# Kernel tuning notes

Hardware: AMD Instinct MI355X
Metric: run time of the kernel (lower is better)

Reference implementation:

```python
import jax, jax.numpy as jnp
import numpy as np
from jax import lax

B, T, H, NC, SKEL, GEN = 512, 256, 512, 512, 256, 16


def setup_inputs() -> dict:
    key = jax.random.key(0)
    ks = jax.random.split(key, 16)
    s = 0.05
    return {
        "inputs": jax.random.randint(ks[0], (B, T), 0, NC),  # teacher-forcing ids (unused, training=False)
        "note_encoded": jax.random.normal(ks[1], (B, SKEL), jnp.float32),
        "genre_cond": jax.random.normal(ks[2], (B, GEN), jnp.float32),
        # hidden_fc
        "W_hid": jax.random.normal(ks[3], (H, SKEL + GEN), jnp.float32) * s,
        "b_hid": jnp.zeros((H,), jnp.float32),
        # embedding table
        "emb": jax.random.normal(ks[4], (NC, H), jnp.float32) * s,
        # gru1 (torch GRUCell layout: gates [r, z, n] stacked along dim 0)
        "W_ih1": jax.random.normal(ks[5], (3 * H, H), jnp.float32) * s,
        "W_hh1": jax.random.normal(ks[6], (3 * H, H), jnp.float32) * s,
        "b_ih1": jnp.zeros((3 * H,), jnp.float32),
        "b_hh1": jnp.zeros((3 * H,), jnp.float32),
        # gru2
        "W_ih2": jax.random.normal(ks[7], (3 * H, H), jnp.float32) * s,
        "W_hh2": jax.random.normal(ks[8], (3 * H, H), jnp.float32) * s,
        "b_ih2": jnp.zeros((3 * H,), jnp.float32),
        "b_hh2": jnp.zeros((3 * H,), jnp.float32),
        # out_fc Linear
        "W_out": jax.random.normal(ks[9], (NC, H), jnp.float32) * s,
        "b_out": jnp.zeros((NC,), jnp.float32),
    }


def gru_cell(x, h, W_ih, W_hh, b_ih, b_hh):
    # torch.nn.GRUCell math
    gi = x @ W_ih.T + b_ih          # [B, 3H]
    gh = h @ W_hh.T + b_hh          # [B, 3H]
    i_r, i_z, i_n = jnp.split(gi, 3, axis=-1)
    h_r, h_z, h_n = jnp.split(gh, 3, axis=-1)
    r = jax.nn.sigmoid(i_r + h_r)
    z = jax.nn.sigmoid(i_z + h_z)
    n = jnp.tanh(i_n + r * h_n)
    return (1.0 - z) * n + z * h


def reference(inputs, note_encoded, genre_cond, W_hid, b_hid, emb,
              W_ih1, W_hh1, b_ih1, b_hh1, W_ih2, W_hh2, b_ih2, b_hh2,
              W_out, b_out):
    batch = note_encoded.shape[0]
    hidden = jnp.concatenate([note_encoded, genre_cond], axis=-1)  # use_genre_cond=True
    h1_init = hidden @ W_hid.T + b_hid                              # [B, H]
    h2_init = jnp.zeros_like(h1_init)  # overwritten at step 0 (hx[1] = hx[0])
    tok0 = jnp.zeros((batch,), jnp.int32)
    sample_keys = jax.random.split(jax.random.key(42), T)

    def step(carry, xs):
        h1, h2, tok = carry
        i, k = xs
        x = emb[tok]                                    # embedding lookup [B, H]
        h1 = gru_cell(x, h1, W_ih1, W_hh1, b_ih1, b_hh1)
        h2_prev = jnp.where(i == 0, h1, h2)             # hx[1] = hx[0] at i==0
        h2 = gru_cell(h1, h2_prev, W_ih2, W_hh2, b_ih2, b_hh2)
        logits = h2 @ W_out.T + b_out                   # [B, NC]
        # Categorical(softmax(logits)/temp) renormalizes => temp is a no-op.
        tok = jax.random.categorical(k, jax.nn.log_softmax(logits, axis=-1)).astype(jnp.int32)
        return (h1, h2, tok), (logits, tok)

    _, (logits_seq, tok_seq) = lax.scan(step, (h1_init, h2_init, tok0),
                                        (jnp.arange(T), sample_keys))
    code_outs = jnp.swapaxes(logits_seq, 0, 1)  # [B, T, NC]
    pred_outs = jnp.swapaxes(tok_seq, 0, 1)     # [B, T]
    return code_outs, pred_outs
```

## Files before the change

kernel.cpp:

```cpp
#include <hip/hip_runtime.h>
#include <stdint.h>

#define BB 512
#define TT 256
#define HH 512
#define NCC 512
#define KIN 272

typedef float v2f __attribute__((ext_vector_type(2)));

__device__ __forceinline__ void tf_round(uint32_t &x0, uint32_t &x1, int r) {
  x0 += x1;
  x1 = (x1 << r) | (x1 >> (32 - r));
  x1 ^= x0;
}

__device__ __forceinline__ void threefry2x32(uint32_t k0, uint32_t k1,
                                             uint32_t c0, uint32_t c1,
                                             uint32_t &o0, uint32_t &o1) {
  uint32_t ks2 = k0 ^ k1 ^ 0x1BD11BDAu;
  uint32_t x0 = c0 + k0, x1 = c1 + k1;
  tf_round(x0, x1, 13); tf_round(x0, x1, 15); tf_round(x0, x1, 26); tf_round(x0, x1, 6);
  x0 += k1;  x1 += ks2 + 1u;
  tf_round(x0, x1, 17); tf_round(x0, x1, 29); tf_round(x0, x1, 16); tf_round(x0, x1, 24);
  x0 += ks2; x1 += k0 + 2u;
  tf_round(x0, x1, 13); tf_round(x0, x1, 15); tf_round(x0, x1, 26); tf_round(x0, x1, 6);
  x0 += k0;  x1 += k1 + 3u;
  tf_round(x0, x1, 17); tf_round(x0, x1, 29); tf_round(x0, x1, 16); tf_round(x0, x1, 24);
  x0 += k1;  x1 += ks2 + 4u;
  tf_round(x0, x1, 13); tf_round(x0, x1, 15); tf_round(x0, x1, 26); tf_round(x0, x1, 6);
  x0 += ks2; x1 += k0 + 5u;
  o0 = x0; o1 = x1;
}

__global__ void __launch_bounds__(256) init_kernel(
    const float* __restrict__ note, const float* __restrict__ genre,
    const float* __restrict__ Whid, const float* __restrict__ bhid,
    const float* __restrict__ emb,
    float* __restrict__ h1T, float* __restrict__ xT, int* __restrict__ tok) {
  int b = blockIdx.x;
  int tid = threadIdx.x;
  __shared__ double u[KIN];
  if (tid < 256) u[tid] = (double)note[b * 256 + tid];
  if (tid < 16)  u[256 + tid] = (double)genre[b * 16 + tid];
  if (tid == 0)  tok[b] = 0;
  __syncthreads();
  for (int j = tid; j < HH; j += 256) {
    double acc = 0.0;
    const float* w = Whid + (size_t)j * KIN;
    #pragma unroll 4
    for (int k = 0; k < KIN; ++k) acc = fma(u[k], (double)w[k], acc);
    h1T[(size_t)j * BB + b] = (float)(acc + (double)bhid[j]);
    xT[(size_t)j * BB + b]  = emb[j];
  }
}

#define CT 8
#define BT 64
#define KT 32
__global__ void __launch_bounds__(256) gru_kernel(
    const float* __restrict__ Wih, const float* __restrict__ Whh,
    const float* __restrict__ bih, const float* __restrict__ bhh,
    const float* __restrict__ hprevT, float* __restrict__ houtT,
    const float* __restrict__ xT) {
  __shared__ float xs[KT][BT];
  __shared__ float hs[KT][BT];
  __shared__ float ws[6][4][KT][2];

  int tid  = threadIdx.x;
  int lane = tid & 63;
  int wv   = tid >> 6;
  int j0   = blockIdx.x * CT;
  int b0   = blockIdx.y * BT;

  int krow = tid >> 3;
  int bq   = (tid & 7) * 8;
  const float* xsrc = xT     + (size_t)krow * BB + b0 + bq;
  const float* hsrc = hprevT + (size_t)krow * BB + b0 + bq;

  auto wsrcf = [&](int f) -> const float* {
    int kq = f & 7, row = f >> 3;
    int cc = row & 1, pr = (row >> 1) & 3, g = row >> 3;
    const float* base = (g < 3) ? Wih : Whh;
    int gg = (g < 3) ? g : g - 3;
    return base + ((size_t)gg * HH + j0 + pr * 2 + cc) * HH + kq * 4;
  };
  auto wdstf = [&](int f) -> float* {
    int kq = f & 7, row = f >> 3;
    int cc = row & 1, pr = (row >> 1) & 3, g = row >> 3;
    return &ws[g][pr][kq * 4][cc];
  };
  bool has2 = (tid < 128);
  const float* wsrc1 = wsrcf(tid);
  const float* wsrc2 = has2 ? wsrcf(tid + 256) : wsrc1;
  float* wdst1 = wdstf(tid);
  float* wdst2 = has2 ? wdstf(tid + 256) : wdst1;

  v2f acc[6];
  #pragma unroll
  for (int g = 0; g < 6; ++g) { acc[g][0] = 0.0f; acc[g][1] = 0.0f; }

  float4 px0 = *(const float4*)(xsrc);
  float4 px1 = *(const float4*)(xsrc + 4);
  float4 ph0 = *(const float4*)(hsrc);
  float4 ph1 = *(const float4*)(hsrc + 4);
  float4 pw1 = *(const float4*)(wsrc1);
  float4 pw2 = *(const float4*)(wsrc2);

  for (int k0 = 0; k0 < HH; k0 += KT) {
    __syncthreads();
    *(float4*)&xs[krow][bq]     = px0;
    *(float4*)&xs[krow][bq + 4] = px1;
    *(float4*)&hs[krow][bq]     = ph0;
    *(float4*)&hs[krow][bq + 4] = ph1;
    wdst1[0] = pw1.x; wdst1[2] = pw1.y; wdst1[4] = pw1.z; wdst1[6] = pw1.w;
    if (has2) { wdst2[0] = pw2.x; wdst2[2] = pw2.y; wdst2[4] = pw2.z; wdst2[6] = pw2.w; }
    __syncthreads();

    if (k0 + KT < HH) {
      xsrc += (size_t)KT * BB; hsrc += (size_t)KT * BB;
      wsrc1 += KT; wsrc2 += KT;
      px0 = *(const float4*)(xsrc);
      px1 = *(const float4*)(xsrc + 4);
      ph0 = *(const float4*)(hsrc);
      ph1 = *(const float4*)(hsrc + 4);
      pw1 = *(const float4*)(wsrc1);
      pw2 = *(const float4*)(wsrc2);
    }

    #pragma unroll 8
    for (int kk = 0; kk < KT; kk += 2) {
      float xa = xs[kk][lane],     ha = hs[kk][lane];
      float xb = xs[kk + 1][lane], hb = hs[kk + 1][lane];
      v2f xa2 = {xa, xa}, xb2 = {xb, xb};
      v2f ha2 = {ha, ha}, hb2 = {hb, hb};
      #pragma unroll
      for (int g = 0; g < 3; ++g) {
        float4 wq = *(const float4*)&ws[g][wv][kk][0];
        v2f lo = {wq.x, wq.y}, hi = {wq.z, wq.w};
        acc[g] = __builtin_elementwise_fma(xa2, lo, acc[g]);
        acc[g] = __builtin_elementwise_fma(xb2, hi, acc[g]);
      }
      #pragma unroll
      for (int g = 3; g < 6; ++g) {
        float4 wq = *(const float4*)&ws[g][wv][kk][0];
        v2f lo = {wq.x, wq.y}, hi = {wq.z, wq.w};
        acc[g] = __builtin_elementwise_fma(ha2, lo, acc[g]);
        acc[g] = __builtin_elementwise_fma(hb2, hi, acc[g]);
      }
    }
  }

  int b = b0 + lane;
  #pragma unroll
  for (int ci = 0; ci < 2; ++ci) {
    int j = j0 + wv * 2 + ci;
    double ir  = (double)acc[0][ci] + (double)bih[j];
    double iz  = (double)acc[1][ci] + (double)bih[HH + j];
    double inn = (double)acc[2][ci] + (double)bih[2 * HH + j];
    double hr  = (double)acc[3][ci] + (double)bhh[j];
    double hz  = (double)acc[4][ci] + (double)bhh[HH + j];
    double hn  = (double)acc[5][ci] + (double)bhh[2 * HH + j];
    double r = 1.0 / (1.0 + exp(-(ir + hr)));
    double z = 1.0 / (1.0 + exp(-(iz + hz)));
    double n = tanh(inn + r * hn);
    double hp = (double)hprevT[(size_t)j * BB + b];
    houtT[(size_t)j * BB + b] = (float)((1.0 - z) * n + z * hp);
  }
}

__global__ void __launch_bounds__(256) sample_kernel(
    const float* __restrict__ Wout, const float* __restrict__ bout,
    const float* __restrict__ h2T, float* __restrict__ out0,
    float* __restrict__ out1, int* __restrict__ tok, int t,
    const float* __restrict__ emb, float* __restrict__ xT) {
  __shared__ double hsh[2][HH];
  __shared__ double rs[2][256];
  __shared__ int    ri[2][256];
  int tid = threadIdx.x;
  int b0 = blockIdx.x * 2;

  for (int i = tid; i < 2 * HH; i += 256)
    hsh[i >> 9][i & 511] = (double)h2T[(size_t)(i & 511) * BB + b0 + (i >> 9)];
  __syncthreads();

  uint32_t k1t, k2t;
  threefry2x32(0u, 42u, 0u, (uint32_t)t, k1t, k2t);

  double sbest[2]; int ibest[2];
  #pragma unroll
  for (int half = 0; half < 2; ++half) {
    int cc = tid + half * 256;
    double acc[2] = {0, 0};
    const float* w = Wout + (size_t)cc * HH;
    for (int k = 0; k < HH; k += 4) {
      float4 wv = *(const float4*)(w + k);
      #pragma unroll
      for (int i = 0; i < 2; ++i) {
        acc[i] = fma(hsh[i][k + 0], (double)wv.x, acc[i]);
        acc[i] = fma(hsh[i][k + 1], (double)wv.y, acc[i]);
        acc[i] = fma(hsh[i][k + 2], (double)wv.z, acc[i]);
        acc[i] = fma(hsh[i][k + 3], (double)wv.w, acc[i]);
      }
    }
    double bo = (double)bout[cc];
    #pragma unroll
    for (int i = 0; i < 2; ++i) {
      int b = b0 + i;
      double lg = acc[i] + bo;
      out0[((size_t)b * TT + t) * NCC + cc] = (float)lg;
      uint32_t o0, o1;
      threefry2x32(k1t, k2t, 0u, (uint32_t)(b * NCC + cc), o0, o1);
      uint32_t bits = o0 ^ o1;
      uint32_t ub = bits >> 9;
      float uf;
      if (ub == 0u) uf = 1.17549435e-38f;
      else          uf = __uint_as_float(0x3f800000u | ub) - 1.0f;
      double g = -log(-log((double)uf));
      double s = lg + g;
      if (half == 0) { sbest[i] = s; ibest[i] = cc; }
      else if (s > sbest[i]) { sbest[i] = s; ibest[i] = cc; }
    }
  }
  #pragma unroll
  for (int i = 0; i < 2; ++i) { rs[i][tid] = sbest[i]; ri[i][tid] = ibest[i]; }
  __syncthreads();
  for (int stride = 128; stride > 0; stride >>= 1) {
    if (tid < stride) {
      #pragma unroll
      for (int i = 0; i < 2; ++i) {
        double so = rs[i][tid + stride]; int io = ri[i][tid + stride];
        double sm = rs[i][tid];          int im = ri[i][tid];
        if (so > sm || (so == sm && io < im)) { rs[i][tid] = so; ri[i][tid] = io; }
      }
    }
    __syncthreads();
  }
  if (tid < 2) {
    int b = b0 + tid;
    int idx = ri[tid][0];
    tok[b] = idx;
    out1[(size_t)b * TT + t] = (float)idx;
  }
  #pragma unroll
  for (int i = 0; i < 2; ++i) {
    int row = ri[i][0];
    int b = b0 + i;
    for (int k = tid; k < HH; k += 256)
      xT[(size_t)k * BB + b] = emb[(size_t)row * HH + k];
  }
}

extern "C" void kernel_launch(void* const* d_in, const int* in_sizes, int n_in,
                              void* d_out, int out_size, void* d_ws, size_t ws_size,
                              hipStream_t stream) {
  const float* note  = (const float*)d_in[1];
  const float* genre = (const float*)d_in[2];
  const float* Whid  = (const float*)d_in[3];
  const float* bhid  = (const float*)d_in[4];
  const float* emb   = (const float*)d_in[5];
  const float* Wih1  = (const float*)d_in[6];
  const float* Whh1  = (const float*)d_in[7];
  const float* bih1  = (const float*)d_in[8];
  const float* bhh1  = (const float*)d_in[9];
  const float* Wih2  = (const float*)d_in[10];
  const float* Whh2  = (const float*)d_in[11];
  const float* bih2  = (const float*)d_in[12];
  const float* bhh2  = (const float*)d_in[13];
  const float* Wout  = (const float*)d_in[14];
  const float* bout  = (const float*)d_in[15];

  float* out0 = (float*)d_out;
  float* out1 = out0 + (size_t)BB * TT * NCC;

  char* wsp = (char*)d_ws;
  float* h1a = (float*)wsp; wsp += (size_t)BB * HH * sizeof(float);
  float* h1b = (float*)wsp; wsp += (size_t)BB * HH * sizeof(float);
  float* h2a = (float*)wsp; wsp += (size_t)BB * HH * sizeof(float);
  float* h2b = (float*)wsp; wsp += (size_t)BB * HH * sizeof(float);
  float* xT  = (float*)wsp; wsp += (size_t)HH * BB * sizeof(float);
  int* tok = (int*)wsp;

  init_kernel<<<BB, 256, 0, stream>>>(note, genre, Whid, bhid, emb, h1a, xT, tok);

  float* c1 = h1a;
  float* c2 = h2a;
  dim3 ggrid(HH / CT, BB / BT);
  for (int t = 0; t < TT; ++t) {
    float* n1 = (c1 == h1a) ? h1b : h1a;
    float* n2 = (c2 == h2a) ? h2b : h2a;
    gru_kernel<<<ggrid, 256, 0, stream>>>(Wih1, Whh1, bih1, bhh1, c1, n1, xT);
    const float* hsrc2 = (t == 0) ? (const float*)n1 : (const float*)c2;
    gru_kernel<<<ggrid, 256, 0, stream>>>(Wih2, Whh2, bih2, bhh2, hsrc2, n2, n1);
    sample_kernel<<<BB / 2, 256, 0, stream>>>(Wout, bout, n2, out0, out1, tok, t,
                                              emb, xT);
    c1 = n1;
    c2 = n2;
  }
}
```

Baseline: 34.59 ms.

## Repack GRU weights per column pair and read them directly from global memory

Adds a repack kernel that lays out the six GRU gate weight matrices as interleaved column pairs, contiguous along k, once per layer at the start of each call. The GRU kernel drops its shared-memory weight staging and reads packed weights straight from global memory with wave-uniform addresses, which should turn into scalar or broadcast loads. This removes the LDS weight stores and their bank traffic. In exchange, weight loads now depend on cache latency inside the inner loop, and two repack launches plus extra workspace are added to every forward call.

```diff
diff --git a/kernel.cpp b/kernel.cpp
--- a/kernel.cpp
+++ b/kernel.cpp
@@ -31,6 +31,20 @@
   tf_round(x0, x1, 13); tf_round(x0, x1, 15); tf_round(x0, x1, 26); tf_round(x0, x1, 6);
   x0 += ks2; x1 += k0 + 5u;
   o0 = x0; o1 = x1;
+}
+
+__global__ void __launch_bounds__(256) repack_kernel(
+    const float* __restrict__ Wih, const float* __restrict__ Whh,
+    float* __restrict__ wpack) {
+  int idx = blockIdx.x * 256 + threadIdx.x;
+  int c   = idx & 1;
+  int k   = (idx >> 1) & 511;
+  int gcp = idx >> 10;
+  int g   = gcp % 6;
+  int cp  = gcp / 6;
+  const float* W = (g < 3) ? Wih : Whh;
+  int gg = (g < 3) ? g : g - 3;
+  wpack[idx] = W[((size_t)(gg * HH + cp * 2 + c)) * HH + k];
 }
 
 __global__ void __launch_bounds__(256) init_kernel(
@@ -55,46 +69,29 @@
   }
 }
 
-#define CT 8
-#define BT 64
-#define KT 32
+#define GBT 64
+#define GKT 32
 __global__ void __launch_bounds__(256) gru_kernel(
-    const float* __restrict__ Wih, const float* __restrict__ Whh,
+    const float* __restrict__ wpack,
     const float* __restrict__ bih, const float* __restrict__ bhh,
     const float* __restrict__ hprevT, float* __restrict__ houtT,
     const float* __restrict__ xT) {
-  __shared__ float xs[KT][BT];
-  __shared__ float hs[KT][BT];
-  __shared__ float ws[6][4][KT][2];
+  __shared__ float xs[GKT][GBT];
+  __shared__ float hs[GKT][GBT];
 
   int tid  = threadIdx.x;
   int lane = tid & 63;
-  int wv   = tid >> 6;
-  int j0   = blockIdx.x * CT;
-  int b0   = blockIdx.y * BT;
-
-  int krow = tid >> 3;
-  int bq   = (tid & 7) * 8;
-  const float* xsrc = xT     + (size_t)krow * BB + b0 + bq;
-  const float* hsrc = hprevT + (size_t)krow * BB + b0 + bq;
-
-  auto wsrcf = [&](int f) -> const float* {
-    int kq = f & 7, row = f >> 3;
-    int cc = row & 1, pr = (row >> 1) & 3, g = row >> 3;
-    const float* base = (g < 3) ? Wih : Whh;
-    int gg = (g < 3) ? g : g - 3;
-    return base + ((size_t)gg * HH + j0 + pr * 2 + cc) * HH + kq * 4;
-  };
-  auto wdstf = [&](int f) -> float* {
-    int kq = f & 7, row = f >> 3;
-    int cc = row & 1, pr = (row >> 1) & 3, g = row >> 3;
-    return &ws[g][pr][kq * 4][cc];
-  };
-  bool has2 = (tid < 128);
-  const float* wsrc1 = wsrcf(tid);
-  const float* wsrc2 = has2 ? wsrcf(tid + 256) : wsrc1;
-  float* wdst1 = wdstf(tid);
-  float* wdst2 = has2 ? wdstf(tid + 256) : wdst1;
+  int wv   = __builtin_amdgcn_readfirstlane(tid >> 6);
+  int j0   = blockIdx.x * 8;
+  int b0   = blockIdx.y * GBT;
+  int cp   = blockIdx.x * 4 + wv;
+
+  const float* wbase = wpack + (size_t)cp * (6 * 512 * 2);
+
+  int kr = tid >> 3;
+  int bq = (tid & 7) * 8;
+  const float* xsrc = xT     + (size_t)kr * BB + b0 + bq;
+  const float* hsrc = hprevT + (size_t)kr * BB + b0 + bq;
 
   v2f acc[6];
   #pragma unroll
@@ -104,46 +101,42 @@
   float4 px1 = *(const float4*)(xsrc + 4);
   float4 ph0 = *(const float4*)(hsrc);
   float4 ph1 = *(const float4*)(hsrc + 4);
-  float4 pw1 = *(const float4*)(wsrc1);
-  float4 pw2 = *(const float4*)(wsrc2);
-
-  for (int k0 = 0; k0 < HH; k0 += KT) {
+
+  for (int k0 = 0; k0 < HH; k0 += GKT) {
     __syncthreads();
-    *(float4*)&xs[krow][bq]     = px0;
-    *(float4*)&xs[krow][bq + 4] = px1;
-    *(float4*)&hs[krow][bq]     = ph0;
-    *(float4*)&hs[krow][bq + 4] = ph1;
-    wdst1[0] = pw1.x; wdst1[2] = pw1.y; wdst1[4] = pw1.z; wdst1[6] = pw1.w;
-    if (has2) { wdst2[0] = pw2.x; wdst2[2] = pw2.y; wdst2[4] = pw2.z; wdst2[6] = pw2.w; }
+    *(float4*)&xs[kr][bq]     = px0;
+    *(float4*)&xs[kr][bq + 4] = px1;
+    *(float4*)&hs[kr][bq]     = ph0;
+    *(float4*)&hs[kr][bq + 4] = ph1;
     __syncthreads();
 
-    if (k0 + KT < HH) {
-      xsrc += (size_t)KT * BB; hsrc += (size_t)KT * BB;
-      wsrc1 += KT; wsrc2 += KT;
+    if (k0 + GKT < HH) {
+      xsrc += (size_t)GKT * BB;
+      hsrc += (size_t)GKT * BB;
       px0 = *(const float4*)(xsrc);
       px1 = *(const float4*)(xsrc + 4);
       ph0 = *(const float4*)(hsrc);
       ph1 = *(const float4*)(hsrc + 4);
-      pw1 = *(const float4*)(wsrc1);
-      pw2 = *(const float4*)(wsrc2);
-    }
-
-    #pragma unroll 8
-    for (int kk = 0; kk < KT; kk += 2) {
+    }
+
+    const float* wk0 = wbase + (size_t)k0 * 2;
+    #pragma unroll
+    for (int kk = 0; kk < GKT; kk += 2) {
       float xa = xs[kk][lane],     ha = hs[kk][lane];
       float xb = xs[kk + 1][lane], hb = hs[kk + 1][lane];
       v2f xa2 = {xa, xa}, xb2 = {xb, xb};
       v2f ha2 = {ha, ha}, hb2 = {hb, hb};
+      const float* wk = wk0 + kk * 2;
       #pragma unroll
       for (int g = 0; g < 3; ++g) {
-        float4 wq = *(const float4*)&ws[g][wv][kk][0];
+        float4 wq = *(const float4*)(wk + g * 1024);
         v2f lo = {wq.x, wq.y}, hi = {wq.z, wq.w};
         acc[g] = __builtin_elementwise_fma(xa2, lo, acc[g]);
         acc[g] = __builtin_elementwise_fma(xb2, hi, acc[g]);
       }
       #pragma unroll
       for (int g = 3; g < 6; ++g) {
-        float4 wq = *(const float4*)&ws[g][wv][kk][0];
+        float4 wq = *(const float4*)(wk + g * 1024);
         v2f lo = {wq.x, wq.y}, hi = {wq.z, wq.w};
         acc[g] = __builtin_elementwise_fma(ha2, lo, acc[g]);
         acc[g] = __builtin_elementwise_fma(hb2, hi, acc[g]);
@@ -279,19 +272,23 @@
   float* h2a = (float*)wsp; wsp += (size_t)BB * HH * sizeof(float);
   float* h2b = (float*)wsp; wsp += (size_t)BB * HH * sizeof(float);
   float* xT  = (float*)wsp; wsp += (size_t)HH * BB * sizeof(float);
+  float* wp1 = (float*)wsp; wsp += (size_t)256 * 6 * 512 * 2 * sizeof(float);
+  float* wp2 = (float*)wsp; wsp += (size_t)256 * 6 * 512 * 2 * sizeof(float);
   int* tok = (int*)wsp;
 
+  repack_kernel<<<12288, 256, 0, stream>>>(Wih1, Whh1, wp1);
+  repack_kernel<<<12288, 256, 0, stream>>>(Wih2, Whh2, wp2);
   init_kernel<<<BB, 256, 0, stream>>>(note, genre, Whid, bhid, emb, h1a, xT, tok);
 
   float* c1 = h1a;
   float* c2 = h2a;
-  dim3 ggrid(HH / CT, BB / BT);
+  dim3 ggrid(HH / 8, BB / GBT);
   for (int t = 0; t < TT; ++t) {
     float* n1 = (c1 == h1a) ? h1b : h1a;
     float* n2 = (c2 == h2a) ? h2b : h2a;
-    gru_kernel<<<ggrid, 256, 0, stream>>>(Wih1, Whh1, bih1, bhh1, c1, n1, xT);
+    gru_kernel<<<ggrid, 256, 0, stream>>>(wp1, bih1, bhh1, c1, n1, xT);
     const float* hsrc2 = (t == 0) ? (const float*)n1 : (const float*)c2;
-    gru_kernel<<<ggrid, 256, 0, stream>>>(Wih2, Whh2, bih2, bhh2, hsrc2, n2, n1);
+    gru_kernel<<<ggrid, 256, 0, stream>>>(wp2, bih2, bhh2, hsrc2, n2, n1);
     sample_kernel<<<BB / 2, 256, 0, stream>>>(Wout, bout, n2, out0, out1, tok, t,
                                               emb, xT);
     c1 = n1;
```

Result: slower. 43.31 ms (+25.2%).
